# Performance work log

Measured on AMD Instinct MI355X. Metric: run time of the kernel, lower is better.

## Reference

```python
import jax, jax.numpy as jnp
import numpy as np

H = 128

def _gine_conv(x, ei, ea, w1, b1, w2, b2):
    # GINEConv (eps=0): out = MLP(x + sum_{j->i} relu(x_j + e_ji))
    src, dst = ei[0], ei[1]
    m = jax.nn.relu(x[src] + ea)                      # [E, H]
    agg = jax.ops.segment_sum(m, dst, num_segments=x.shape[0])
    h = x + agg
    return jax.nn.relu(h @ w1 + b1) @ w2 + b2

def _bn(x, gamma, beta, eps=1e-5):
    # BatchNorm1d over node dim, batch statistics (training mode)
    mu = jnp.mean(x, axis=0)
    var = jnp.mean((x - mu) ** 2, axis=0)
    return gamma * (x - mu) * jax.lax.rsqrt(var + eps) + beta

def _scatter_mean(vals, ids, mask, n):
    w = mask.astype(vals.dtype)
    s = jax.ops.segment_sum(vals * w[:, None], ids, num_segments=n)
    c = jax.ops.segment_sum(w, ids, num_segments=n)
    return s / jnp.maximum(c, 1.0)[:, None]


def setup_inputs() -> dict:
    key = jax.random.key(0)
    ks = jax.random.split(key, 20)
    Nf, Nt, S, K = 320000, 100000, 20000, 16
    Ei, Eg = 1280000, 800000
    sc = 1.0 / np.sqrt(H)
    inp = {}
    inp["h_flat"] = jax.random.normal(ks[0], (Nf, H), jnp.float32)
    inp["intra_ei"] = jax.random.randint(ks[1], (2, Ei), 0, Nf, jnp.int32)
    inp["ea_flat"] = jax.random.normal(ks[2], (Ei, H), jnp.float32)
    inp["valid"] = jnp.ones((Nf,), jnp.bool_)
    inp["node_ids"] = jax.random.randint(ks[3], (Nf,), 0, Nt, jnp.int32)
    inp["N_total"] = Nt
    inp["edge_index"] = jax.random.randint(ks[4], (2, Eg), 0, Nt, jnp.int32)
    inp["edge_attr"] = jax.random.normal(ks[5], (Eg, H), jnp.float32)
    inp["sub_batch"] = jax.random.randint(ks[6], (Nf,), 0, S, jnp.int32)
    inp["S"] = S
    inp["k"] = K
    inp["root_flat_idx"] = jax.random.randint(ks[7], (S,), 0, Nf, jnp.int32)
    inp["is_root"] = jnp.zeros((Nf,), jnp.bool_)
    # parameters
    inp["local_w1"] = jax.random.normal(ks[8], (H, H), jnp.float32) * sc
    inp["local_b1"] = jnp.zeros((H,), jnp.float32)
    inp["local_w2"] = jax.random.normal(ks[9], (H, H), jnp.float32) * sc
    inp["local_b2"] = jnp.zeros((H,), jnp.float32)
    inp["local_gamma"] = jnp.ones((H,), jnp.float32)
    inp["local_beta"] = jnp.zeros((H,), jnp.float32)
    inp["global_w1"] = jax.random.normal(ks[10], (H, H), jnp.float32) * sc
    inp["global_b1"] = jnp.zeros((H,), jnp.float32)
    inp["global_w2"] = jax.random.normal(ks[11], (H, H), jnp.float32) * sc
    inp["global_b2"] = jnp.zeros((H,), jnp.float32)
    inp["global_gamma"] = jnp.ones((H,), jnp.float32)
    inp["global_beta"] = jnp.zeros((H,), jnp.float32)
    inp["skip_w"] = jax.random.normal(ks[12], (H, H), jnp.float32) * sc
    inp["skip_b"] = jnp.zeros((H,), jnp.float32)
    inp["vv_w"] = jax.random.normal(ks[13], (H, H), jnp.float32) * sc
    inp["vv_b"] = jnp.zeros((H,), jnp.float32)
    inp["kk_w"] = jax.random.normal(ks[14], (H, H), jnp.float32) * sc
    inp["kk_b"] = jnp.zeros((H,), jnp.float32)
    return inp


def reference(h_flat, intra_ei, ea_flat, valid, node_ids, N_total, edge_index, edge_attr,
              sub_batch, S, k, root_flat_idx, is_root,
              local_w1, local_b1, local_w2, local_b2, local_gamma, local_beta,
              global_w1, global_b1, global_w2, global_b2, global_gamma, global_beta,
              skip_w, skip_b, vv_w, vv_b, kk_w, kk_b):
    valid_f = valid.astype(h_flat.dtype)[:, None]
    clamped_ids = jnp.maximum(node_ids, 0)
    valid_mask = node_ids >= 0

    h_skip = (h_flat @ skip_w + skip_b) * valid_f

    h1 = _gine_conv(h_flat, intra_ei, ea_flat, local_w1, local_b1, local_w2, local_b2)
    h1 = _bn(h1, local_gamma, local_beta) * valid_f

    x_sum = _scatter_mean(h_flat, clamped_ids, valid_mask, N_total)   # [N_total, H]
    h2 = _gine_conv(x_sum, edge_index, edge_attr, global_w1, global_b1, global_w2, global_b2)
    h2 = _bn(h2, global_gamma, global_beta)[clamped_ids] * valid_f

    root_ids = node_ids[root_flat_idx]
    root_valid = root_ids >= 0
    x_vv_canonical = _scatter_mean(h_flat[root_flat_idx], jnp.maximum(root_ids, 0), root_valid, N_total)
    x_vv = (x_vv_canonical[clamped_ids] @ vv_w + vv_b) * valid_f

    x_kk = (h_flat[root_flat_idx[sub_batch]] @ kk_w + kk_b) * valid_f

    out = jax.nn.relu(h_skip + h1 + h2 + x_vv + x_kk)
    # dropout p=0.0 -> identity
    return out * valid_f
```

## Files before the change

kernel.cpp:

```cpp
#include <hip/hip_runtime.h>

#define H    128
#define HQ   32
#define TM   64
#define NT   100000
#define XS   136


typedef __attribute__((ext_vector_type(8))) short short8;
typedef __attribute__((ext_vector_type(4))) float f32x4;

static __host__ int cdiv(long a, long b) { return (int)((a + b - 1) / b); }
static __host__ char* alignp(char* p) {
    return (char*)(((uintptr_t)p + 255) & ~(uintptr_t)255);
}

__device__ inline unsigned short f2bf(float f) {
    unsigned u = __float_as_uint(f);
    unsigned r = u + 0x7FFFu + ((u >> 16) & 1u);
    return (unsigned short)(r >> 16);
}
__device__ inline float bf2f(unsigned short u) {
    return __uint_as_float((unsigned)u << 16);
}

struct WJobs { const float* src[7]; };

__global__ __launch_bounds__(256) void k_cvt_all(
    const float* __restrict__ in, unsigned short* __restrict__ out, long n8,
    WJobs wj, unsigned short* __restrict__ dstBase, int nCvt)
{
    if ((int)blockIdx.x < nCvt) {
        long i = (long)blockIdx.x * 256 + threadIdx.x;
        if (i >= n8) return;
        float4 a = ((const float4*)in)[2 * i];
        float4 b = ((const float4*)in)[2 * i + 1];
        ushort4 lo; lo.x = f2bf(a.x); lo.y = f2bf(a.y); lo.z = f2bf(a.z); lo.w = f2bf(a.w);
        ushort4 hi; hi.x = f2bf(b.x); hi.y = f2bf(b.y); hi.z = f2bf(b.z); hi.w = f2bf(b.w);
        ((ushort4*)out)[2 * i]     = lo;
        ((ushort4*)out)[2 * i + 1] = hi;
    } else {
        int b = blockIdx.x - nCvt;
        int w = b >> 4, chunk = b & 15;
        int i = chunk * 256 + threadIdx.x;
        int k = i >> 5, n4 = (i & 31) * 4;
        float4 v = ((const float4*)wj.src[w])[i];
        unsigned short* dst = dstBase + (size_t)w * H * H;
        dst[(n4 + 0) * H + k] = f2bf(v.x);
        dst[(n4 + 1) * H + k] = f2bf(v.y);
        dst[(n4 + 2) * H + k] = f2bf(v.z);
        dst[(n4 + 3) * H + k] = f2bf(v.w);
    }
}

struct CsrJobs {
    const int* ids[4];
    const int* rfi;
    int* cnt[4];
    int* rp[4];
    int* cur[4];
    int* eid[4];
    int  E[4];
    int  N[4];
    int  histBase[5];
    int  scanBase[5];
};

__device__ inline int csr_id(const CsrJobs& jb, int sg, int e)
{
    if (sg == 3) {
        int nid = jb.ids[2][jb.rfi[e]];
        return nid > 0 ? nid : 0;
    }
    return jb.ids[sg][e];
}

__global__ __launch_bounds__(256) void k_hist4(CsrJobs jb)
{
    int b = blockIdx.x, sg = 0;
    while (b >= jb.histBase[sg + 1]) ++sg;
    int e = (b - jb.histBase[sg]) * 256 + threadIdx.x;
    if (e < jb.E[sg]) atomicAdd(&jb.cnt[sg][csr_id(jb, sg, e)], 1);
}

__global__ __launch_bounds__(256) void k_scanA4(CsrJobs jb, int* __restrict__ parts)
{
    int b = blockIdx.x, sg = 0;
    while (b >= jb.scanBase[sg + 1]) ++sg;
    int lb = b - jb.scanBase[sg];
    const int* cnt = jb.cnt[sg];
    int* rowptr = jb.rp[sg];
    int N = jb.N[sg];
    int* partials = parts + sg * 256;

    __shared__ int lsum[256];
    int tid = threadIdx.x;
    int base = lb * 2048 + tid * 8;
    int v[8];
    int tsum = 0;
#pragma unroll
    for (int i = 0; i < 8; ++i) {
        int idx = base + i;
        int t = (idx < N) ? cnt[idx] : 0;
        v[i] = tsum;
        tsum += t;
    }
    lsum[tid] = tsum;
    __syncthreads();
    for (int off = 1; off < 256; off <<= 1) {
        int t = (tid >= off) ? lsum[tid - off] : 0;
        __syncthreads();
        lsum[tid] += t;
        __syncthreads();
    }
    int texcl = lsum[tid] - tsum;
#pragma unroll
    for (int i = 0; i < 8; ++i) {
        int idx = base + i;
        if (idx < N) rowptr[idx] = v[i] + texcl;
    }
    if (tid == 255) partials[lb] = lsum[255];
}

__global__ __launch_bounds__(256) void k_scanB4(CsrJobs jb, int* __restrict__ parts)
{
    int sg = blockIdx.x;
    int P = jb.scanBase[sg + 1] - jb.scanBase[sg];
    int* partials = parts + sg * 256;
    int* rowptr = jb.rp[sg];
    int N = jb.N[sg];

    __shared__ int lsum[256];
    int tid = threadIdx.x;
    int val = (tid < P) ? partials[tid] : 0;
    lsum[tid] = val;
    __syncthreads();
    for (int off = 1; off < 256; off <<= 1) {
        int t = (tid >= off) ? lsum[tid - off] : 0;
        __syncthreads();
        lsum[tid] += t;
        __syncthreads();
    }
    if (tid < P) partials[tid] = lsum[tid] - val;
    if (tid == 255) rowptr[N] = lsum[255];
}

__global__ __launch_bounds__(256) void k_scanC4(CsrJobs jb, const int* __restrict__ parts)
{
    int b = blockIdx.x, sg = 0;
    while (b >= jb.scanBase[sg + 1]) ++sg;
    int lb = b - jb.scanBase[sg];
    int off = parts[sg * 256 + lb];
    int N = jb.N[sg];
    int* rowptr = jb.rp[sg];
    int* cursor = jb.cur[sg];
    int base = lb * 2048;
    for (int i = threadIdx.x; i < 2048; i += 256) {
        int g = base + i;
        if (g < N) {
            int v = rowptr[g] + off;
            rowptr[g] = v;
            cursor[g] = v;
        }
    }
}

__global__ __launch_bounds__(256) void k_fillperm4(CsrJobs jb)
{
    int b = blockIdx.x, sg = 0;
    while (b >= jb.histBase[sg + 1]) ++sg;
    int e = (b - jb.histBase[sg]) * 256 + threadIdx.x;
    if (e < jb.E[sg]) {
        int pos = atomicAdd(&jb.cur[sg][csr_id(jb, sg, e)], 1);
        jb.eid[sg][pos] = e;
    }
}

__global__ __launch_bounds__(256) void k_csr_mean(
    const unsigned short* __restrict__ X, const int* __restrict__ eid,
    const int* __restrict__ rowptr, unsigned short* __restrict__ OUT, int N)
{
    int idx = blockIdx.x * 256 + threadIdx.x;
    int n = idx >> 5, l = idx & 31;
    if (n >= N) return;
    int beg = rowptr[n], end = rowptr[n + 1];
    float4 acc = {0.f, 0.f, 0.f, 0.f};
    for (int c0 = beg; c0 < end; c0 += 32) {
        int cnt = min(32, end - c0);
        int f_l = 0;
        if (l < cnt) f_l = eid[c0 + l];
        for (int j = 0; j < cnt; ++j) {
            int fi = __shfl(f_l, j, 32);
            ushort4 h = ((const ushort4*)(X + (size_t)fi * H))[l];
            acc.x += bf2f(h.x); acc.y += bf2f(h.y);
            acc.z += bf2f(h.z); acc.w += bf2f(h.w);
        }
    }
    float inv = 1.0f / fmaxf((float)(end - beg), 1.0f);
    ushort4 o;
    o.x = f2bf(acc.x * inv); o.y = f2bf(acc.y * inv);
    o.z = f2bf(acc.z * inv); o.w = f2bf(acc.w * inv);
    ((ushort4*)(OUT + (size_t)n * H))[l] = o;
}

__device__ inline void stage_x_copy(
    unsigned short* sX, const unsigned short* X1, const int* gidx,
    int r0, int M, int tid)
{
    int r = tid >> 2, q = tid & 3;
    int row = r0 + r;
    unsigned short* dst = &sX[r * XS + q * 32];
    if (row < M) {
        int sr = gidx ? gidx[row] : row;
        const ushort4* xp = (const ushort4*)(X1 + (size_t)sr * H + q * 32);
#pragma unroll
        for (int i = 0; i < 8; ++i) *(ushort4*)(dst + i * 4) = xp[i];
    } else {
#pragma unroll
        for (int i = 0; i < 8; ++i) *(ushort4*)(dst + i * 4) = ushort4{0, 0, 0, 0};
    }
}

__device__ inline void stage_x_agg(
    unsigned short* sX, const unsigned short* X1, const float* EA,
    const int* src, const int* eid, const int* rowptr,
    int r0, int M, int tid)
{
    int r = tid >> 2, q = tid & 3;
    int row = r0 + r;
    unsigned short* dst = &sX[r * XS + q * 32];
    if (row < M) {
        float4 m[8];
        const ushort4* xp = (const ushort4*)(X1 + (size_t)row * H + q * 32);
#pragma unroll
        for (int i = 0; i < 8; ++i) {
            ushort4 v = xp[i];
            m[i].x = bf2f(v.x); m[i].y = bf2f(v.y);
            m[i].z = bf2f(v.z); m[i].w = bf2f(v.w);
        }
        int beg = rowptr[row], end = rowptr[row + 1];
        for (int j = beg; j < end; ++j) {
            int e = eid[j];
            int s = src[e];
            const float4* ep = (const float4*)(EA + (size_t)e * H) + q * 8;
            const ushort4* hp = (const ushort4*)(X1 + (size_t)s * H + q * 32);
#pragma unroll
            for (int i = 0; i < 8; ++i) {
                float4 a = ep[i];
                ushort4 h = hp[i];
                m[i].x += fmaxf(bf2f(h.x) + a.x, 0.f);
                m[i].y += fmaxf(bf2f(h.y) + a.y, 0.f);
                m[i].z += fmaxf(bf2f(h.z) + a.z, 0.f);
                m[i].w += fmaxf(bf2f(h.w) + a.w, 0.f);
            }
        }
#pragma unroll
        for (int i = 0; i < 8; ++i) {
            ushort4 b;
            b.x = f2bf(m[i].x); b.y = f2bf(m[i].y);
            b.z = f2bf(m[i].z); b.w = f2bf(m[i].w);
            *(ushort4*)(dst + i * 4) = b;
        }
    } else {
#pragma unroll
        for (int i = 0; i < 8; ++i) *(ushort4*)(dst + i * 4) = ushort4{0, 0, 0, 0};
    }
}

__device__ inline void stage_wt_pre(
    unsigned short* sWT, const unsigned short* WT, int tid)
{
    for (int i = tid; i < H * HQ; i += 256) {
        int n = i >> 5, kq = i & 31;
        *(ushort4*)&sWT[n * XS + kq * 4] = ((const ushort4*)WT)[i];
    }
}

__global__ __launch_bounds__(256) void k_gemm(
    const unsigned short* __restrict__ X1, const int* __restrict__ gidx,
    const unsigned short* __restrict__ WT, const float* __restrict__ B,
    unsigned short* __restrict__ OUT, int M)
{
    __shared__ unsigned short sX[TM * XS];
    __shared__ unsigned short sWT[H * XS];
    __shared__ float sB[H];
    int tid = threadIdx.x;
    int r0 = blockIdx.x * TM;

    stage_x_copy(sX, X1, gidx, r0, M, tid);
    stage_wt_pre(sWT, WT, tid);
    if (tid < 32) ((float4*)sB)[tid] = ((const float4*)B)[tid];
    __syncthreads();

    int wv = tid >> 6, l = tid & 63;
    int lr = l & 15, hi = l >> 4, lk = hi * 8;

    f32x4 acc[8];
#pragma unroll
    for (int ct = 0; ct < 8; ++ct) acc[ct] = {0.f, 0.f, 0.f, 0.f};
#pragma unroll
    for (int kk = 0; kk < 4; ++kk) {
        short8 a = *(const short8*)&sX[(wv * 16 + lr) * XS + kk * 32 + lk];
#pragma unroll
        for (int ct = 0; ct < 8; ++ct) {
            short8 b = *(const short8*)&sWT[(ct * 16 + lr) * XS + kk * 32 + lk];
            acc[ct] = __builtin_amdgcn_mfma_f32_16x16x32_bf16(a, b, acc[ct], 0, 0, 0);
        }
    }

    int orow0 = r0 + wv * 16 + hi * 4;
#pragma unroll
    for (int ct = 0; ct < 8; ++ct) {
        int col = ct * 16 + lr;
        float bias = sB[col];
#pragma unroll
        for (int j = 0; j < 4; ++j) {
            int row = orow0 + j;
            if (row >= M) continue;
            OUT[(size_t)row * H + col] = f2bf(acc[ct][j] + bias);
        }
    }
}

__global__ __launch_bounds__(256) void k_mean_gemm(
    const unsigned short* __restrict__ X, const int* __restrict__ eid,
    const int* __restrict__ rowmap, const int* __restrict__ rowptr,
    const unsigned short* __restrict__ WT, const float* __restrict__ B,
    unsigned short* __restrict__ OUT, int M)
{
    __shared__ unsigned short sX[TM * XS];
    __shared__ unsigned short sWT[H * XS];
    __shared__ float sB[H];
    int tid = threadIdx.x;
    int r0 = blockIdx.x * TM;

    {
        int r = tid >> 2, q = tid & 3;
        int row = r0 + r;
        float4 m[8];
#pragma unroll
        for (int i = 0; i < 8; ++i) m[i] = {0.f, 0.f, 0.f, 0.f};
        int cnt = 0;
        if (row < M) {
            int beg = rowptr[row], end = rowptr[row + 1];
            cnt = end - beg;
            for (int j = beg; j < end; ++j) {
                int fi = rowmap[eid[j]];
                const ushort4* hp = (const ushort4*)(X + (size_t)fi * H + q * 32);
#pragma unroll
                for (int i = 0; i < 8; ++i) {
                    ushort4 v = hp[i];
                    m[i].x += bf2f(v.x); m[i].y += bf2f(v.y);
                    m[i].z += bf2f(v.z); m[i].w += bf2f(v.w);
                }
            }
        }
        float inv = 1.0f / fmaxf((float)cnt, 1.0f);
        unsigned short* dst = &sX[r * XS + q * 32];
#pragma unroll
        for (int i = 0; i < 8; ++i) {
            ushort4 b;
            b.x = f2bf(m[i].x * inv); b.y = f2bf(m[i].y * inv);
            b.z = f2bf(m[i].z * inv); b.w = f2bf(m[i].w * inv);
            *(ushort4*)(dst + i * 4) = b;
        }
    }
    stage_wt_pre(sWT, WT, tid);
    if (tid < 32) ((float4*)sB)[tid] = ((const float4*)B)[tid];
    __syncthreads();

    int wv = tid >> 6, l = tid & 63;
    int lr = l & 15, hi = l >> 4, lk = hi * 8;

    f32x4 acc[8];
#pragma unroll
    for (int ct = 0; ct < 8; ++ct) acc[ct] = {0.f, 0.f, 0.f, 0.f};
#pragma unroll
    for (int kk = 0; kk < 4; ++kk) {
        short8 a = *(const short8*)&sX[(wv * 16 + lr) * XS + kk * 32 + lk];
#pragma unroll
        for (int ct = 0; ct < 8; ++ct) {
            short8 b = *(const short8*)&sWT[(ct * 16 + lr) * XS + kk * 32 + lk];
            acc[ct] = __builtin_amdgcn_mfma_f32_16x16x32_bf16(a, b, acc[ct], 0, 0, 0);
        }
    }

    int orow0 = r0 + wv * 16 + hi * 4;
#pragma unroll
    for (int ct = 0; ct < 8; ++ct) {
        int col = ct * 16 + lr;
        float bias = sB[col];
#pragma unroll
        for (int j = 0; j < 4; ++j) {
            int row = orow0 + j;
            if (row >= M) continue;
            OUT[(size_t)row * H + col] = f2bf(acc[ct][j] + bias);
        }
    }
}

__global__ __launch_bounds__(256) void k_mlp_agg(
    const unsigned short* __restrict__ X1,
    const float* __restrict__ EA, const int* __restrict__ src,
    const int* __restrict__ eid, const int* __restrict__ rowptr,
    const unsigned short* __restrict__ W1T, const float* __restrict__ B1,
    const unsigned short* __restrict__ W2T, const float* __restrict__ B2,
    unsigned short* __restrict__ OUT, int M,
    float* __restrict__ gs, float* __restrict__ gs2)
{
    __shared__ unsigned short sX[TM * XS];
    __shared__ unsigned short sWT[H * XS];
    __shared__ float sB1[H], sB2[H];
    __shared__ float sS[H], sS2[H];
    int tid = threadIdx.x;
    int r0 = blockIdx.x * TM;

    stage_x_agg(sX, X1, EA, src, eid, rowptr, r0, M, tid);
    stage_wt_pre(sWT, W1T, tid);
    if (tid < 32) ((float4*)sB1)[tid] = ((const float4*)B1)[tid];
    else if (tid < 64) ((float4*)sB2)[tid - 32] = ((const float4*)B2)[tid - 32];
    if (tid >= 64 && tid < 192) { sS[tid - 64] = 0.f; sS2[tid - 64] = 0.f; }
    __syncthreads();

    int wv = tid >> 6, l = tid & 63;
    int lr = l & 15, hi = l >> 4, lk = hi * 8;
    int rloc = wv * 16 + hi * 4;

    f32x4 acc[8];
#pragma unroll
    for (int ct = 0; ct < 8; ++ct) acc[ct] = {0.f, 0.f, 0.f, 0.f};
#pragma unroll
    for (int kk = 0; kk < 4; ++kk) {
        short8 a = *(const short8*)&sX[(wv * 16 + lr) * XS + kk * 32 + lk];
#pragma unroll
        for (int ct = 0; ct < 8; ++ct) {
            short8 b = *(const short8*)&sWT[(ct * 16 + lr) * XS + kk * 32 + lk];
            acc[ct] = __builtin_amdgcn_mfma_f32_16x16x32_bf16(a, b, acc[ct], 0, 0, 0);
        }
    }
    __syncthreads();

#pragma unroll
    for (int ct = 0; ct < 8; ++ct) {
        int c = ct * 16 + lr;
        float b1v = sB1[c];
#pragma unroll
        for (int j = 0; j < 4; ++j) {
            float v = fmaxf(acc[ct][j] + b1v, 0.f);
            int mybf = (int)f2bf(v);
            int other = __shfl_xor(mybf, 1);
            if (!(lr & 1)) {
                unsigned packed = (unsigned)(unsigned short)mybf
                                | ((unsigned)(unsigned short)other << 16);
                *(unsigned*)&sX[(rloc + j) * XS + c] = packed;
            }
        }
        acc[ct] = {0.f, 0.f, 0.f, 0.f};
    }
    stage_wt_pre(sWT, W2T, tid);
    __syncthreads();

#pragma unroll
    for (int kk = 0; kk < 4; ++kk) {
        short8 a = *(const short8*)&sX[(wv * 16 + lr) * XS + kk * 32 + lk];
#pragma unroll
        for (int ct = 0; ct < 8; ++ct) {
            short8 b = *(const short8*)&sWT[(ct * 16 + lr) * XS + kk * 32 + lk];
            acc[ct] = __builtin_amdgcn_mfma_f32_16x16x32_bf16(a, b, acc[ct], 0, 0, 0);
        }
    }

    int orow0 = r0 + rloc;
#pragma unroll
    for (int ct = 0; ct < 8; ++ct) {
        int col = ct * 16 + lr;
        float b2v = sB2[col];
        float ps = 0.f, ps2 = 0.f;
#pragma unroll
        for (int j = 0; j < 4; ++j) {
            int row = orow0 + j;
            if (row >= M) continue;
            float o = acc[ct][j] + b2v;
            OUT[(size_t)row * H + col] = f2bf(o);
            ps += o; ps2 += o * o;
        }
        atomicAdd(&sS[col], ps);
        atomicAdd(&sS2[col], ps2);
    }
    __syncthreads();
    if (tid < H) {
        unsafeAtomicAdd(&gs[tid], sS[tid]);
        unsafeAtomicAdd(&gs2[tid], sS2[tid]);
    }
}

__global__ __launch_bounds__(256) void k_final_gemm(
    const unsigned short* __restrict__ Hf,
    const unsigned short* __restrict__ SKWT, const float* __restrict__ SKB,
    const unsigned short* __restrict__ h1raw, const unsigned short* __restrict__ h2raw,
    const unsigned short* __restrict__ vvy, const unsigned short* __restrict__ kky,
    const int* __restrict__ node_ids, const int* __restrict__ sub_batch,
    const float* __restrict__ stats,
    const float* __restrict__ lg, const float* __restrict__ lbe,
    const float* __restrict__ gg, const float* __restrict__ gbe,
    float n1, float n2,
    float* __restrict__ OUT, int M)
{
    __shared__ unsigned short sX[TM * XS];
    __shared__ unsigned short sWT[H * XS];
    __shared__ float sP[5 * H];
    int tid = threadIdx.x;
    int r0 = blockIdx.x * TM;

    stage_x_copy(sX, Hf, nullptr, r0, M, tid);
    stage_wt_pre(sWT, SKWT, tid);
    if (tid < H) {
        float mu = stats[tid] / n1;
        float var = stats[H + tid] / n1 - mu * mu;
        float sc = lg[tid] * rsqrtf(var + 1e-5f);
        sP[tid] = sc; sP[H + tid] = lbe[tid] - mu * sc;
        mu = stats[2 * H + tid] / n2;
        var = stats[3 * H + tid] / n2 - mu * mu;
        sc = gg[tid] * rsqrtf(var + 1e-5f);
        sP[2 * H + tid] = sc; sP[3 * H + tid] = gbe[tid] - mu * sc;
    } else if (tid < H + 32) {
        ((float4*)(sP + 4 * H))[tid - H] = ((const float4*)SKB)[tid - H];
    }
    __syncthreads();

    int wv = tid >> 6, l = tid & 63;
    int lr = l & 15, hi = l >> 4, lk = hi * 8;

    f32x4 acc[8];
#pragma unroll
    for (int ct = 0; ct < 8; ++ct) acc[ct] = {0.f, 0.f, 0.f, 0.f};
#pragma unroll
    for (int kk = 0; kk < 4; ++kk) {
        short8 a = *(const short8*)&sX[(wv * 16 + lr) * XS + kk * 32 + lk];
#pragma unroll
        for (int ct = 0; ct < 8; ++ct) {
            short8 b = *(const short8*)&sWT[(ct * 16 + lr) * XS + kk * 32 + lk];
            acc[ct] = __builtin_amdgcn_mfma_f32_16x16x32_bf16(a, b, acc[ct], 0, 0, 0);
        }
    }
    __syncthreads();

    float* sF = (float*)sWT;
    int rloc0 = wv * 16 + hi * 4;
#pragma unroll
    for (int ct = 0; ct < 8; ++ct) {
        int col = ct * 16 + lr;
        float skbv = sP[4 * H + col];
#pragma unroll
        for (int j = 0; j < 4; ++j)
            sF[(rloc0 + j) * 130 + col] = acc[ct][j] + skbv;
    }
    __syncthreads();

    {
        int r = tid >> 2, q = tid & 3;
        int row = r0 + r;
        if (row < M) {
            int nid = node_ids[row];
            size_t cid = (size_t)(nid > 0 ? nid : 0);
            size_t sb  = (size_t)sub_batch[row];
            const ushort4* h1p = (const ushort4*)(h1raw + (size_t)row * H + q * 32);
            const ushort4* h2p = (const ushort4*)(h2raw + cid * H + q * 32);
            const ushort4* vvp = (const ushort4*)(vvy + cid * H + q * 32);
            const ushort4* kkp = (const ushort4*)(kky + sb * H + q * 32);
            float* op = OUT + (size_t)row * H + q * 32;
            const float* fr = &sF[r * 130 + q * 32];
#pragma unroll
            for (int i = 0; i < 8; ++i) {
                ushort4 a = h1p[i], b = h2p[i], c = vvp[i], d = kkp[i];
                int cb = q * 32 + i * 4;
                float4 o;
                o.x = fr[i * 4 + 0] + bf2f(a.x) * sP[cb + 0] + sP[H + cb + 0]
                    + bf2f(b.x) * sP[2 * H + cb + 0] + sP[3 * H + cb + 0]
                    + bf2f(c.x) + bf2f(d.x);
                o.y = fr[i * 4 + 1] + bf2f(a.y) * sP[cb + 1] + sP[H + cb + 1]
                    + bf2f(b.y) * sP[2 * H + cb + 1] + sP[3 * H + cb + 1]
                    + bf2f(c.y) + bf2f(d.y);
                o.z = fr[i * 4 + 2] + bf2f(a.z) * sP[cb + 2] + sP[H + cb + 2]
                    + bf2f(b.z) * sP[2 * H + cb + 2] + sP[3 * H + cb + 2]
                    + bf2f(c.z) + bf2f(d.z);
                o.w = fr[i * 4 + 3] + bf2f(a.w) * sP[cb + 3] + sP[H + cb + 3]
                    + bf2f(b.w) * sP[2 * H + cb + 3] + sP[3 * H + cb + 3]
                    + bf2f(c.w) + bf2f(d.w);
                o.x = fmaxf(o.x, 0.f); o.y = fmaxf(o.y, 0.f);
                o.z = fmaxf(o.z, 0.f); o.w = fmaxf(o.w, 0.f);
                ((float4*)op)[i] = o;
            }
        }
    }
}

extern "C" void kernel_launch(void* const* d_in, const int* in_sizes, int n_in,
                              void* d_out, int out_size, void* d_ws, size_t ws_size,
                              hipStream_t stream)
{
    const float* h_flat        = (const float*)d_in[0];
    const int*   intra_ei      = (const int*)d_in[1];
    const float* ea_flat       = (const float*)d_in[2];
    const int*   node_ids      = (const int*)d_in[4];
    const int*   edge_index    = (const int*)d_in[6];
    const float* edge_attr     = (const float*)d_in[7];
    const int*   sub_batch     = (const int*)d_in[8];
    const int*   root_flat_idx = (const int*)d_in[11];
    const float* lw1 = (const float*)d_in[13];
    const float* lb1 = (const float*)d_in[14];
    const float* lw2 = (const float*)d_in[15];
    const float* lb2 = (const float*)d_in[16];
    const float* lg  = (const float*)d_in[17];
    const float* lbe = (const float*)d_in[18];
    const float* gw1 = (const float*)d_in[19];
    const float* gb1 = (const float*)d_in[20];
    const float* gw2 = (const float*)d_in[21];
    const float* gb2 = (const float*)d_in[22];
    const float* gg  = (const float*)d_in[23];
    const float* gbe = (const float*)d_in[24];
    const float* skw = (const float*)d_in[25];
    const float* skb = (const float*)d_in[26];
    const float* vvw = (const float*)d_in[27];
    const float* vvb = (const float*)d_in[28];
    const float* kkw = (const float*)d_in[29];
    const float* kkb = (const float*)d_in[30];

    const int Nf = in_sizes[0] / H;
    const int Ei = in_sizes[2] / H;
    const int Eg = in_sizes[7] / H;
    const int S  = in_sizes[11];

    char* w = (char*)d_ws;
    unsigned short* hbf  = (unsigned short*)w; w += (size_t)Nf * H * 2;
    unsigned short* buf1 = (unsigned short*)w; w += (size_t)Nf * H * 2;
    unsigned short* xsum = (unsigned short*)w; w += (size_t)NT * H * 2;
    unsigned short* buf2 = (unsigned short*)w; w += (size_t)NT * H * 2;
    unsigned short* vvy  = (unsigned short*)w; w += (size_t)NT * H * 2;
    unsigned short* kbuf = (unsigned short*)w; w += (size_t)S * H * 2;
    unsigned short* wtb  = (unsigned short*)w; w += (size_t)7 * H * H * 2;
    w = alignp(w);
    int* cntAll = (int*)w; w += ((size_t)Nf + 3 * (size_t)NT) * 4;
    float* stats = (float*)w; w += 4 * H * 4;
    w = alignp(w);
    int* rpA  = (int*)w; w += ((size_t)Nf + 1) * 4;  w = alignp(w);
    int* rpB  = (int*)w; w += ((size_t)NT + 1) * 4;  w = alignp(w);
    int* rpC  = (int*)w; w += ((size_t)NT + 1) * 4;  w = alignp(w);
    int* rpD  = (int*)w; w += ((size_t)NT + 1) * 4;  w = alignp(w);
    int* curA = (int*)w; w += (size_t)Nf * 4;
    int* curB = (int*)w; w += (size_t)NT * 4;
    int* curC = (int*)w; w += (size_t)NT * 4;
    int* curD = (int*)w; w += (size_t)NT * 4;
    int* eidA = (int*)w; w += (size_t)Ei * 4;
    int* eidB = (int*)w; w += (size_t)Eg * 4;
    int* eidC = (int*)w; w += (size_t)Nf * 4;
    int* eidD = (int*)w; w += (size_t)S * 4;
    int* parts = (int*)w; w += 4 * 256 * 4;
    int* cntA = cntAll;
    int* cntB = cntA + Nf;
    int* cntC = cntB + NT;
    int* cntD = cntC + NT;

    hipMemsetAsync(cntAll, 0, ((size_t)Nf + 3 * (size_t)NT) * 4 + 4 * H * 4, stream);

    WJobs wj;
    wj.src[0] = lw1; wj.src[1] = lw2; wj.src[2] = gw1; wj.src[3] = gw2;
    wj.src[4] = skw; wj.src[5] = vvw; wj.src[6] = kkw;
    int nCvt = cdiv((long)Nf * H / 8, 256);
    k_cvt_all<<<nCvt + 7 * 16, 256, 0, stream>>>(
        h_flat, hbf, (long)Nf * H / 8, wj, wtb, nCvt);

    CsrJobs jb;
    jb.ids[0] = intra_ei + Ei;  jb.ids[1] = edge_index + Eg;
    jb.ids[2] = node_ids;       jb.ids[3] = nullptr;
    jb.rfi = root_flat_idx;
    jb.cnt[0] = cntA; jb.cnt[1] = cntB; jb.cnt[2] = cntC; jb.cnt[3] = cntD;
    jb.rp[0]  = rpA;  jb.rp[1]  = rpB;  jb.rp[2]  = rpC;  jb.rp[3]  = rpD;
    jb.cur[0] = curA; jb.cur[1] = curB; jb.cur[2] = curC; jb.cur[3] = curD;
    jb.eid[0] = eidA; jb.eid[1] = eidB; jb.eid[2] = eidC; jb.eid[3] = eidD;
    jb.E[0] = Ei; jb.E[1] = Eg; jb.E[2] = Nf; jb.E[3] = S;
    jb.N[0] = Nf; jb.N[1] = NT; jb.N[2] = NT; jb.N[3] = NT;
    jb.histBase[0] = 0;
    for (int i = 0; i < 4; ++i) jb.histBase[i + 1] = jb.histBase[i] + cdiv(jb.E[i], 256);
    jb.scanBase[0] = 0;
    for (int i = 0; i < 4; ++i) jb.scanBase[i + 1] = jb.scanBase[i] + cdiv(jb.N[i], 2048);

    k_hist4<<<jb.histBase[4], 256, 0, stream>>>(jb);
    k_scanA4<<<jb.scanBase[4], 256, 0, stream>>>(jb, parts);
    k_scanB4<<<4, 256, 0, stream>>>(jb, parts);
    k_scanC4<<<jb.scanBase[4], 256, 0, stream>>>(jb, parts);
    k_fillperm4<<<jb.histBase[4], 256, 0, stream>>>(jb);

    k_csr_mean<<<cdiv((long)NT * 32, 256), 256, 0, stream>>>(
        hbf, eidC, rpC, xsum, NT);

    k_mlp_agg<<<cdiv(Nf, TM), 256, 0, stream>>>(
        hbf, ea_flat, intra_ei, eidA, rpA,
        wtb + 0 * H * H, lb1, wtb + 1 * H * H, lb2,
        buf1, Nf, stats, stats + H);
    k_mlp_agg<<<cdiv(NT, TM), 256, 0, stream>>>(
        xsum, edge_attr, edge_index, eidB, rpB,
        wtb + 2 * H * H, gb1, wtb + 3 * H * H, gb2,
        buf2, NT, stats + 2 * H, stats + 3 * H);

    k_mean_gemm<<<cdiv(NT, TM), 256, 0, stream>>>(
        hbf, eidD, root_flat_idx, rpD, wtb + 5 * H * H, vvb, vvy, NT);
    k_gemm<<<cdiv(S, TM), 256, 0, stream>>>(hbf, root_flat_idx,
                                            wtb + 6 * H * H, kkb, kbuf, S);

    k_final_gemm<<<cdiv(Nf, TM), 256, 0, stream>>>(
        hbf, wtb + 4 * H * H, skb, buf1, buf2, vvy, kbuf, node_ids, sub_batch,
        stats, lg, lbe, gg, gbe, (float)Nf, (float)NT, (float*)d_out, Nf);
}
```

Measured before the change: 1.264 ms.

## Distribute edge aggregation across block threads with LDS float atomics

The edge aggregation in k_mlp_agg no longer gives one thread-quarter a whole destination row's edge list. Instead, all edges of the block's 64-row tile are spread across groups of 8 threads, which accumulate relu(x_src+ea) into a float LDS buffer (aliased onto the weight tile) with atomicAdd. The goal is to remove load imbalance from variable degree and to expose more memory parallelism on the gathers. The cost is LDS atomic traffic, extra syncs, serialising the weight staging after aggregation, and non-deterministic summation order.

New measurement: 2.359 ms. +86.6%, slower.

```diff
diff --git a/kernel.cpp b/kernel.cpp
--- a/kernel.cpp
+++ b/kernel.cpp
@@ -5,6 +5,7 @@
 #define TM   64
 #define NT   100000
 #define XS   136
+#define AS   130
 
 
 typedef __attribute__((ext_vector_type(8))) short short8;
@@ -221,52 +222,6 @@
     }
 }
 
-__device__ inline void stage_x_agg(
-    unsigned short* sX, const unsigned short* X1, const float* EA,
-    const int* src, const int* eid, const int* rowptr,
-    int r0, int M, int tid)
-{
-    int r = tid >> 2, q = tid & 3;
-    int row = r0 + r;
-    unsigned short* dst = &sX[r * XS + q * 32];
-    if (row < M) {
-        float4 m[8];
-        const ushort4* xp = (const ushort4*)(X1 + (size_t)row * H + q * 32);
-#pragma unroll
-        for (int i = 0; i < 8; ++i) {
-            ushort4 v = xp[i];
-            m[i].x = bf2f(v.x); m[i].y = bf2f(v.y);
-            m[i].z = bf2f(v.z); m[i].w = bf2f(v.w);
-        }
-        int beg = rowptr[row], end = rowptr[row + 1];
-        for (int j = beg; j < end; ++j) {
-            int e = eid[j];
-            int s = src[e];
-            const float4* ep = (const float4*)(EA + (size_t)e * H) + q * 8;
-            const ushort4* hp = (const ushort4*)(X1 + (size_t)s * H + q * 32);
-#pragma unroll
-            for (int i = 0; i < 8; ++i) {
-                float4 a = ep[i];
-                ushort4 h = hp[i];
-                m[i].x += fmaxf(bf2f(h.x) + a.x, 0.f);
-                m[i].y += fmaxf(bf2f(h.y) + a.y, 0.f);
-                m[i].z += fmaxf(bf2f(h.z) + a.z, 0.f);
-                m[i].w += fmaxf(bf2f(h.w) + a.w, 0.f);
-            }
-        }
-#pragma unroll
-        for (int i = 0; i < 8; ++i) {
-            ushort4 b;
-            b.x = f2bf(m[i].x); b.y = f2bf(m[i].y);
-            b.z = f2bf(m[i].z); b.w = f2bf(m[i].w);
-            *(ushort4*)(dst + i * 4) = b;
-        }
-    } else {
-#pragma unroll
-        for (int i = 0; i < 8; ++i) *(ushort4*)(dst + i * 4) = ushort4{0, 0, 0, 0};
-    }
-}
-
 __device__ inline void stage_wt_pre(
     unsigned short* sWT, const unsigned short* WT, int tid)
 {
@@ -402,6 +357,7 @@
 __global__ __launch_bounds__(256) void k_mlp_agg(
     const unsigned short* __restrict__ X1,
     const float* __restrict__ EA, const int* __restrict__ src,
+    const int* __restrict__ dst,
     const int* __restrict__ eid, const int* __restrict__ rowptr,
     const unsigned short* __restrict__ W1T, const float* __restrict__ B1,
     const unsigned short* __restrict__ W2T, const float* __restrict__ B2,
@@ -414,12 +370,72 @@
     __shared__ float sS[H], sS2[H];
     int tid = threadIdx.x;
     int r0 = blockIdx.x * TM;
-
-    stage_x_agg(sX, X1, EA, src, eid, rowptr, r0, M, tid);
-    stage_wt_pre(sWT, W1T, tid);
+    float* sAcc = (float*)sWT;
+
+    {
+        int r = tid >> 2, q = tid & 3;
+        int row = r0 + r;
+        float* ap = &sAcc[r * AS + q * 32];
+        if (row < M) {
+            const ushort4* xp = (const ushort4*)(X1 + (size_t)row * H + q * 32);
+#pragma unroll
+            for (int i = 0; i < 8; ++i) {
+                ushort4 v = xp[i];
+                ap[i * 4 + 0] = bf2f(v.x); ap[i * 4 + 1] = bf2f(v.y);
+                ap[i * 4 + 2] = bf2f(v.z); ap[i * 4 + 3] = bf2f(v.w);
+            }
+        } else {
+#pragma unroll
+            for (int i = 0; i < 8; ++i) {
+                ap[i * 4 + 0] = 0.f; ap[i * 4 + 1] = 0.f;
+                ap[i * 4 + 2] = 0.f; ap[i * 4 + 3] = 0.f;
+            }
+        }
+    }
     if (tid < 32) ((float4*)sB1)[tid] = ((const float4*)B1)[tid];
     else if (tid < 64) ((float4*)sB2)[tid - 32] = ((const float4*)B2)[tid - 32];
     if (tid >= 64 && tid < 192) { sS[tid - 64] = 0.f; sS2[tid - 64] = 0.f; }
+    __syncthreads();
+
+    {
+        int rend = min(r0 + TM, M);
+        int begB = rowptr[r0], endB = rowptr[rend];
+        int q8 = tid & 7;
+        for (int j = begB + (tid >> 3); j < endB; j += 32) {
+            int e = eid[j];
+            int rr = dst[e] - r0;
+            int s = src[e];
+            const float4* ep = (const float4*)(EA + (size_t)e * H) + q8 * 4;
+            const ushort4* hp = (const ushort4*)(X1 + (size_t)s * H + q8 * 16);
+            float* ap = &sAcc[rr * AS + q8 * 16];
+#pragma unroll
+            for (int i = 0; i < 4; ++i) {
+                float4 a = ep[i];
+                ushort4 h = hp[i];
+                atomicAdd(ap + i * 4 + 0, fmaxf(bf2f(h.x) + a.x, 0.f));
+                atomicAdd(ap + i * 4 + 1, fmaxf(bf2f(h.y) + a.y, 0.f));
+                atomicAdd(ap + i * 4 + 2, fmaxf(bf2f(h.z) + a.z, 0.f));
+                atomicAdd(ap + i * 4 + 3, fmaxf(bf2f(h.w) + a.w, 0.f));
+            }
+        }
+    }
+    __syncthreads();
+
+    {
+        int r = tid >> 2, q = tid & 3;
+        const float* ap = &sAcc[r * AS + q * 32];
+        unsigned short* dp = &sX[r * XS + q * 32];
+#pragma unroll
+        for (int i = 0; i < 8; ++i) {
+            ushort4 b;
+            b.x = f2bf(ap[i * 4 + 0]); b.y = f2bf(ap[i * 4 + 1]);
+            b.z = f2bf(ap[i * 4 + 2]); b.w = f2bf(ap[i * 4 + 3]);
+            *(ushort4*)(dp + i * 4) = b;
+        }
+    }
+    __syncthreads();
+
+    stage_wt_pre(sWT, W1T, tid);
     __syncthreads();
 
     int wv = tid >> 6, l = tid & 63;
@@ -695,11 +711,11 @@
         hbf, eidC, rpC, xsum, NT);
 
     k_mlp_agg<<<cdiv(Nf, TM), 256, 0, stream>>>(
-        hbf, ea_flat, intra_ei, eidA, rpA,
+        hbf, ea_flat, intra_ei, intra_ei + Ei, eidA, rpA,
         wtb + 0 * H * H, lb1, wtb + 1 * H * H, lb2,
         buf1, Nf, stats, stats + H);
     k_mlp_agg<<<cdiv(NT, TM), 256, 0, stream>>>(
-        xsum, edge_attr, edge_index, eidB, rpB,
+        xsum, edge_attr, edge_index, edge_index + Eg, eidB, rpB,
         wtb + 2 * H * H, gb1, wtb + 3 * H * H, gb2,
         buf2, NT, stats + 2 * H, stats + 3 * H);
 
```

## Precompute CSR-ordered source ids, unroll edge gather, halve weight LDS in MLP kernel

Applied to the files above, without the earlier changes.

The CSR fill step now also writes the source node of each edge in CSR order, so the aggregation loop no longer does a dependent src[eid] gather. The edge loop is unrolled by two to keep more independent loads in flight. The weight tile in shared memory is cut to half size and loaded in two passes, which lowers LDS use per block so more blocks can be resident. The cost is extra syncs and weight reloads per GEMM, plus a larger CSR workspace and extra writes during the fill.

Measured after the change: 1.122 ms, median of 2. 11.3% less time.

```diff
diff --git a/kernel.cpp b/kernel.cpp
--- a/kernel.cpp
+++ b/kernel.cpp
@@ -55,11 +55,13 @@
 
 struct CsrJobs {
     const int* ids[4];
+    const int* srcarr[4];
     const int* rfi;
     int* cnt[4];
     int* rp[4];
     int* cur[4];
     int* eid[4];
+    int* srcv[4];
     int  E[4];
     int  N[4];
     int  histBase[5];
@@ -173,6 +175,7 @@
     if (e < jb.E[sg]) {
         int pos = atomicAdd(&jb.cur[sg][csr_id(jb, sg, e)], 1);
         jb.eid[sg][pos] = e;
+        if (jb.srcarr[sg]) jb.srcv[sg][pos] = jb.srcarr[sg][e];
     }
 }
 
@@ -221,58 +224,21 @@
     }
 }
 
-__device__ inline void stage_x_agg(
-    unsigned short* sX, const unsigned short* X1, const float* EA,
-    const int* src, const int* eid, const int* rowptr,
-    int r0, int M, int tid)
-{
-    int r = tid >> 2, q = tid & 3;
-    int row = r0 + r;
-    unsigned short* dst = &sX[r * XS + q * 32];
-    if (row < M) {
-        float4 m[8];
-        const ushort4* xp = (const ushort4*)(X1 + (size_t)row * H + q * 32);
-#pragma unroll
-        for (int i = 0; i < 8; ++i) {
-            ushort4 v = xp[i];
-            m[i].x = bf2f(v.x); m[i].y = bf2f(v.y);
-            m[i].z = bf2f(v.z); m[i].w = bf2f(v.w);
-        }
-        int beg = rowptr[row], end = rowptr[row + 1];
-        for (int j = beg; j < end; ++j) {
-            int e = eid[j];
-            int s = src[e];
-            const float4* ep = (const float4*)(EA + (size_t)e * H) + q * 8;
-            const ushort4* hp = (const ushort4*)(X1 + (size_t)s * H + q * 32);
-#pragma unroll
-            for (int i = 0; i < 8; ++i) {
-                float4 a = ep[i];
-                ushort4 h = hp[i];
-                m[i].x += fmaxf(bf2f(h.x) + a.x, 0.f);
-                m[i].y += fmaxf(bf2f(h.y) + a.y, 0.f);
-                m[i].z += fmaxf(bf2f(h.z) + a.z, 0.f);
-                m[i].w += fmaxf(bf2f(h.w) + a.w, 0.f);
-            }
-        }
-#pragma unroll
-        for (int i = 0; i < 8; ++i) {
-            ushort4 b;
-            b.x = f2bf(m[i].x); b.y = f2bf(m[i].y);
-            b.z = f2bf(m[i].z); b.w = f2bf(m[i].w);
-            *(ushort4*)(dst + i * 4) = b;
-        }
-    } else {
-#pragma unroll
-        for (int i = 0; i < 8; ++i) *(ushort4*)(dst + i * 4) = ushort4{0, 0, 0, 0};
-    }
-}
-
 __device__ inline void stage_wt_pre(
     unsigned short* sWT, const unsigned short* WT, int tid)
 {
     for (int i = tid; i < H * HQ; i += 256) {
         int n = i >> 5, kq = i & 31;
         *(ushort4*)&sWT[n * XS + kq * 4] = ((const ushort4*)WT)[i];
+    }
+}
+
+__device__ inline void stage_wt_half(
+    unsigned short* sWT, const unsigned short* WT, int h, int tid)
+{
+    for (int i = tid; i < 64 * HQ; i += 256) {
+        int n = i >> 5, kq = i & 31;
+        *(ushort4*)&sWT[n * XS + kq * 4] = ((const ushort4*)WT)[h * 2048 + i];
     }
 }
 
@@ -401,22 +367,81 @@
 
 __global__ __launch_bounds__(256) void k_mlp_agg(
     const unsigned short* __restrict__ X1,
-    const float* __restrict__ EA, const int* __restrict__ src,
-    const int* __restrict__ eid, const int* __restrict__ rowptr,
+    const float* __restrict__ EA,
+    const int* __restrict__ eid, const int* __restrict__ srcv,
+    const int* __restrict__ rowptr,
     const unsigned short* __restrict__ W1T, const float* __restrict__ B1,
     const unsigned short* __restrict__ W2T, const float* __restrict__ B2,
     unsigned short* __restrict__ OUT, int M,
     float* __restrict__ gs, float* __restrict__ gs2)
 {
     __shared__ unsigned short sX[TM * XS];
-    __shared__ unsigned short sWT[H * XS];
+    __shared__ unsigned short sWT[64 * XS];
     __shared__ float sB1[H], sB2[H];
     __shared__ float sS[H], sS2[H];
     int tid = threadIdx.x;
     int r0 = blockIdx.x * TM;
 
-    stage_x_agg(sX, X1, EA, src, eid, rowptr, r0, M, tid);
-    stage_wt_pre(sWT, W1T, tid);
+    {
+        int r = tid >> 2, q = tid & 3;
+        int row = r0 + r;
+        unsigned short* dst = &sX[r * XS + q * 32];
+        if (row < M) {
+            float4 m[8];
+            const ushort4* xp = (const ushort4*)(X1 + (size_t)row * H + q * 32);
+#pragma unroll
+            for (int i = 0; i < 8; ++i) {
+                ushort4 v = xp[i];
+                m[i].x = bf2f(v.x); m[i].y = bf2f(v.y);
+                m[i].z = bf2f(v.z); m[i].w = bf2f(v.w);
+            }
+            int beg = rowptr[row], end = rowptr[row + 1];
+            int j = beg;
+            for (; j + 2 <= end; j += 2) {
+                int e0 = eid[j], e1 = eid[j + 1];
+                int s0 = srcv[j], s1 = srcv[j + 1];
+                const float4* ep0 = (const float4*)(EA + (size_t)e0 * H) + q * 8;
+                const float4* ep1 = (const float4*)(EA + (size_t)e1 * H) + q * 8;
+                const ushort4* hp0 = (const ushort4*)(X1 + (size_t)s0 * H + q * 32);
+                const ushort4* hp1 = (const ushort4*)(X1 + (size_t)s1 * H + q * 32);
+#pragma unroll
+                for (int i = 0; i < 8; ++i) {
+                    float4 a0 = ep0[i], a1 = ep1[i];
+                    ushort4 h0 = hp0[i], h1 = hp1[i];
+                    m[i].x += fmaxf(bf2f(h0.x) + a0.x, 0.f) + fmaxf(bf2f(h1.x) + a1.x, 0.f);
+                    m[i].y += fmaxf(bf2f(h0.y) + a0.y, 0.f) + fmaxf(bf2f(h1.y) + a1.y, 0.f);
+                    m[i].z += fmaxf(bf2f(h0.z) + a0.z, 0.f) + fmaxf(bf2f(h1.z) + a1.z, 0.f);
+                    m[i].w += fmaxf(bf2f(h0.w) + a0.w, 0.f) + fmaxf(bf2f(h1.w) + a1.w, 0.f);
+                }
+            }
+            if (j < end) {
+                int e = eid[j];
+                int s = srcv[j];
+                const float4* ep = (const float4*)(EA + (size_t)e * H) + q * 8;
+                const ushort4* hp = (const ushort4*)(X1 + (size_t)s * H + q * 32);
+#pragma unroll
+                for (int i = 0; i < 8; ++i) {
+                    float4 a = ep[i];
+                    ushort4 h = hp[i];
+                    m[i].x += fmaxf(bf2f(h.x) + a.x, 0.f);
+                    m[i].y += fmaxf(bf2f(h.y) + a.y, 0.f);
+                    m[i].z += fmaxf(bf2f(h.z) + a.z, 0.f);
+                    m[i].w += fmaxf(bf2f(h.w) + a.w, 0.f);
+                }
+            }
+#pragma unroll
+            for (int i = 0; i < 8; ++i) {
+                ushort4 b;
+                b.x = f2bf(m[i].x); b.y = f2bf(m[i].y);
+                b.z = f2bf(m[i].z); b.w = f2bf(m[i].w);
+                *(ushort4*)(dst + i * 4) = b;
+            }
+        } else {
+#pragma unroll
+            for (int i = 0; i < 8; ++i) *(ushort4*)(dst + i * 4) = ushort4{0, 0, 0, 0};
+        }
+    }
+    stage_wt_half(sWT, W1T, 0, tid);
     if (tid < 32) ((float4*)sB1)[tid] = ((const float4*)B1)[tid];
     else if (tid < 64) ((float4*)sB2)[tid - 32] = ((const float4*)B2)[tid - 32];
     if (tid >= 64 && tid < 192) { sS[tid - 64] = 0.f; sS2[tid - 64] = 0.f; }
@@ -429,12 +454,25 @@
     f32x4 acc[8];
 #pragma unroll
     for (int ct = 0; ct < 8; ++ct) acc[ct] = {0.f, 0.f, 0.f, 0.f};
+
 #pragma unroll
     for (int kk = 0; kk < 4; ++kk) {
         short8 a = *(const short8*)&sX[(wv * 16 + lr) * XS + kk * 32 + lk];
 #pragma unroll
-        for (int ct = 0; ct < 8; ++ct) {
+        for (int ct = 0; ct < 4; ++ct) {
             short8 b = *(const short8*)&sWT[(ct * 16 + lr) * XS + kk * 32 + lk];
+            acc[ct] = __builtin_amdgcn_mfma_f32_16x16x32_bf16(a, b, acc[ct], 0, 0, 0);
+        }
+    }
+    __syncthreads();
+    stage_wt_half(sWT, W1T, 1, tid);
+    __syncthreads();
+#pragma unroll
+    for (int kk = 0; kk < 4; ++kk) {
+        short8 a = *(const short8*)&sX[(wv * 16 + lr) * XS + kk * 32 + lk];
+#pragma unroll
+        for (int ct = 4; ct < 8; ++ct) {
+            short8 b = *(const short8*)&sWT[((ct - 4) * 16 + lr) * XS + kk * 32 + lk];
             acc[ct] = __builtin_amdgcn_mfma_f32_16x16x32_bf16(a, b, acc[ct], 0, 0, 0);
         }
     }
@@ -457,15 +495,27 @@
         }
         acc[ct] = {0.f, 0.f, 0.f, 0.f};
     }
-    stage_wt_pre(sWT, W2T, tid);
+    stage_wt_half(sWT, W2T, 0, tid);
     __syncthreads();
 
 #pragma unroll
     for (int kk = 0; kk < 4; ++kk) {
         short8 a = *(const short8*)&sX[(wv * 16 + lr) * XS + kk * 32 + lk];
 #pragma unroll
-        for (int ct = 0; ct < 8; ++ct) {
+        for (int ct = 0; ct < 4; ++ct) {
             short8 b = *(const short8*)&sWT[(ct * 16 + lr) * XS + kk * 32 + lk];
+            acc[ct] = __builtin_amdgcn_mfma_f32_16x16x32_bf16(a, b, acc[ct], 0, 0, 0);
+        }
+    }
+    __syncthreads();
+    stage_wt_half(sWT, W2T, 1, tid);
+    __syncthreads();
+#pragma unroll
+    for (int kk = 0; kk < 4; ++kk) {
+        short8 a = *(const short8*)&sX[(wv * 16 + lr) * XS + kk * 32 + lk];
+#pragma unroll
+        for (int ct = 4; ct < 8; ++ct) {
+            short8 b = *(const short8*)&sWT[((ct - 4) * 16 + lr) * XS + kk * 32 + lk];
             acc[ct] = __builtin_amdgcn_mfma_f32_16x16x32_bf16(a, b, acc[ct], 0, 0, 0);
         }
     }
@@ -655,6 +705,8 @@
     int* eidB = (int*)w; w += (size_t)Eg * 4;
     int* eidC = (int*)w; w += (size_t)Nf * 4;
     int* eidD = (int*)w; w += (size_t)S * 4;
+    int* srcvA = (int*)w; w += (size_t)Ei * 4;
+    int* srcvB = (int*)w; w += (size_t)Eg * 4;
     int* parts = (int*)w; w += 4 * 256 * 4;
     int* cntA = cntAll;
     int* cntB = cntA + Nf;
@@ -673,11 +725,14 @@
     CsrJobs jb;
     jb.ids[0] = intra_ei + Ei;  jb.ids[1] = edge_index + Eg;
     jb.ids[2] = node_ids;       jb.ids[3] = nullptr;
+    jb.srcarr[0] = intra_ei;    jb.srcarr[1] = edge_index;
+    jb.srcarr[2] = nullptr;     jb.srcarr[3] = nullptr;
     jb.rfi = root_flat_idx;
     jb.cnt[0] = cntA; jb.cnt[1] = cntB; jb.cnt[2] = cntC; jb.cnt[3] = cntD;
     jb.rp[0]  = rpA;  jb.rp[1]  = rpB;  jb.rp[2]  = rpC;  jb.rp[3]  = rpD;
     jb.cur[0] = curA; jb.cur[1] = curB; jb.cur[2] = curC; jb.cur[3] = curD;
     jb.eid[0] = eidA; jb.eid[1] = eidB; jb.eid[2] = eidC; jb.eid[3] = eidD;
+    jb.srcv[0] = srcvA; jb.srcv[1] = srcvB; jb.srcv[2] = nullptr; jb.srcv[3] = nullptr;
     jb.E[0] = Ei; jb.E[1] = Eg; jb.E[2] = Nf; jb.E[3] = S;
     jb.N[0] = Nf; jb.N[1] = NT; jb.N[2] = NT; jb.N[3] = NT;
     jb.histBase[0] = 0;
@@ -695,11 +750,11 @@
         hbf, eidC, rpC, xsum, NT);
 
     k_mlp_agg<<<cdiv(Nf, TM), 256, 0, stream>>>(
-        hbf, ea_flat, intra_ei, eidA, rpA,
+        hbf, ea_flat, eidA, srcvA, rpA,
         wtb + 0 * H * H, lb1, wtb + 1 * H * H, lb2,
         buf1, Nf, stats, stats + H);
     k_mlp_agg<<<cdiv(NT, TM), 256, 0, stream>>>(
-        xsum, edge_attr, edge_index, eidB, rpB,
+        xsum, edge_attr, eidB, srcvB, rpB,
         wtb + 2 * H * H, gb1, wtb + 3 * H * H, gb2,
         buf2, NT, stats + 2 * H, stats + 3 * H);
 
```
